# Performance work log

Hardware: AMD Instinct MI355X
Metric: run time of the kernel (lower is better)

Reference implementation:

```python
import jax, jax.numpy as jnp
import numpy as np

N = 50000
E = 800000
IN_F = 128
HID = 128
OUT_F = 64
MU = 2.0
EPS = 1e-12


def setup_inputs() -> dict:
    key = jax.random.key(0)
    ks = jax.random.split(key, 20)
    d = {}
    d["x"] = jax.random.normal(ks[0], (N, IN_F), dtype=jnp.float32)
    d["edge_src"] = jax.random.randint(ks[1], (E,), 0, N, dtype=jnp.int32)
    d["edge_dst"] = jax.random.randint(ks[2], (E,), 0, N, dtype=jnp.int32)
    d["edge_val"] = jax.random.uniform(ks[3], (E,), dtype=jnp.float32)
    # layer 0: in=128 -> pool=128 -> out=128 (activation=relu)
    s0 = 1.0 / np.sqrt(IN_F)
    d["pool_w0"] = jax.random.uniform(ks[4], (IN_F, IN_F), jnp.float32, -s0, s0)
    d["pool_b0"] = jax.random.uniform(ks[5], (IN_F,), jnp.float32, -s0, s0)
    d["fc1_w0"] = jax.random.uniform(ks[6], (HID, IN_F), jnp.float32, -s0, s0)
    d["fc1_b0"] = jax.random.uniform(ks[7], (HID,), jnp.float32, -s0, s0)
    d["fc2_w0"] = jax.random.uniform(ks[8], (HID, IN_F), jnp.float32, -s0, s0)
    d["fc2_b0"] = jax.random.uniform(ks[9], (HID,), jnp.float32, -s0, s0)
    # layer 1 (final): in=128 -> pool=128 -> out=64 (no activation)
    s1 = 1.0 / np.sqrt(HID)
    d["pool_w1"] = jax.random.uniform(ks[10], (HID, HID), jnp.float32, -s1, s1)
    d["pool_b1"] = jax.random.uniform(ks[11], (HID,), jnp.float32, -s1, s1)
    d["fc1_w1"] = jax.random.uniform(ks[12], (OUT_F, HID), jnp.float32, -s1, s1)
    d["fc1_b1"] = jax.random.uniform(ks[13], (OUT_F,), jnp.float32, -s1, s1)
    d["fc2_w1"] = jax.random.uniform(ks[14], (OUT_F, HID), jnp.float32, -s1, s1)
    d["fc2_b1"] = jax.random.uniform(ks[15], (OUT_F,), jnp.float32, -s1, s1)
    return d


def _sage_conv(x, src, dst, val, pw, pb, w1, b1, w2, b2, act):
    # L2-normalize rows (F.normalize(x, dim=1))
    xn = x / jnp.maximum(jnp.linalg.norm(x, axis=1, keepdims=True), EPS)
    h = jax.nn.relu(xn @ pw.T + pb)               # [N, pool]
    h_mu = h ** MU                                # elementwise pow
    # spmm(adj, h_mu): gather source rows, scale by edge weight, scatter-add to dst rows
    agg = jax.ops.segment_sum(h_mu[src] * val[:, None], dst, num_segments=N)
    agg = agg ** (1.0 / MU)                       # generalized-mean root
    out = (h @ w1.T + b1) + (agg @ w2.T + b2)
    return jax.nn.relu(out) if act else out


def reference(x, edge_src, edge_dst, edge_val,
              pool_w0, pool_b0, fc1_w0, fc1_b0, fc2_w0, fc2_b0,
              pool_w1, pool_b1, fc1_w1, fc1_b1, fc2_w1, fc2_b1):
    h = _sage_conv(x, edge_src, edge_dst, edge_val,
                   pool_w0, pool_b0, fc1_w0, fc1_b0, fc2_w0, fc2_b0, act=True)
    out = _sage_conv(h, edge_src, edge_dst, edge_val,
                     pool_w1, pool_b1, fc1_w1, fc1_b1, fc2_w1, fc2_b1, act=False)
    return out
```

## Files before the change

### kernel.cpp

```cpp
#include <hip/hip_runtime.h>

#define FF 128
#define BCAP 8192
#define CHUNK 4096
#define PITCH 136

typedef __attribute__((ext_vector_type(8))) short short8;
typedef __attribute__((ext_vector_type(4))) float f32x4;

__device__ __forceinline__ unsigned short bf16_rne(float f) {
    unsigned u = __float_as_uint(f);
    u += 0x7fffu + ((u >> 16) & 1u);
    return (unsigned short)(u >> 16);
}
__device__ __forceinline__ float bf16_to_f32(unsigned short h) {
    return __uint_as_float(((unsigned)h) << 16);
}

__global__ __launch_bounds__(256, 2)
void poolpartA_kernel(const float* __restrict__ x,
                      const unsigned short* __restrict__ Wh, const unsigned short* __restrict__ Wl,
                      const float* __restrict__ bias,
                      unsigned short* __restrict__ hout, unsigned short* __restrict__ hsqout,
                      const int* __restrict__ esrc, const int* __restrict__ edst,
                      const float* __restrict__ eval,
                      int* __restrict__ bucket_cnt, int2* __restrict__ ebuf,
                      int N, int E, int nchunks)
{
    __shared__ alignas(16) char smem[37888];
    const int t = threadIdx.x;

    if (blockIdx.x < nchunks) {
        int* cnt   = (int*)smem;
        int* sc    = cnt + 256;
        int* excl  = sc + 256;
        int* cur   = excl + 256;
        int* gbase = cur + 256;
        int2* staged = (int2*)(smem + 5 * 256 * 4);
        const int e0 = blockIdx.x * CHUNK;
        const int n  = min(CHUNK, E - e0);

        cnt[t] = 0;
        __syncthreads();
        for (int i = t; i < n; i += 256)
            atomicAdd(&cnt[((unsigned)edst[e0 + i]) >> 8], 1);
        __syncthreads();

        sc[t] = cnt[t];
        __syncthreads();
        #pragma unroll
        for (int off = 1; off < 256; off <<= 1) {
            int v = (t >= off) ? sc[t - off] : 0;
            __syncthreads();
            sc[t] += v;
            __syncthreads();
        }
        excl[t] = sc[t] - cnt[t];
        cur[t]  = excl[t];
        if (cnt[t] > 0) gbase[t] = atomicAdd(&bucket_cnt[t], cnt[t]);
        __syncthreads();

        for (int i = t; i < n; i += 256) {
            int d = edst[e0 + i];
            int s = esrc[e0 + i];
            float v = eval[e0 + i];
            int b = ((unsigned)d) >> 8;
            int slot = atomicAdd(&cur[b], 1);
            staged[slot] = make_int2((s & 0xffff) | (d << 16), __float_as_int(v));
        }
        __syncthreads();

        for (int p = t; p < n; p += 256) {
            int2 ent = staged[p];
            int b = ((unsigned)ent.x) >> 24;
            int gpos = gbase[b] + (p - excl[b]);
            ebuf[(size_t)b * BCAP + gpos] = ent;
        }
    } else {
        unsigned short* sX = (unsigned short*)smem;
        float* sNorm = (float*)(smem + 64 * PITCH * 2);
        unsigned short* sOutQ = (unsigned short*)(smem + 64 * PITCH * 2 + 256);
        const int tile = blockIdx.x - nchunks;

        #pragma unroll
        for (int rg = 0; rg < 2; ++rg) {
            const int row = rg * 32 + (t >> 3);
            const int c0  = (t & 7) * 16;
            const int n   = tile * 64 + row;
            const int base = row * PITCH + c0;
            float v[16];
            if (n < N) {
                const float4* p = (const float4*)(x + (size_t)n * FF + c0);
                #pragma unroll
                for (int i = 0; i < 4; ++i) {
                    float4 q = p[i];
                    v[4*i] = q.x; v[4*i+1] = q.y; v[4*i+2] = q.z; v[4*i+3] = q.w;
                }
            } else {
                #pragma unroll
                for (int i = 0; i < 16; ++i) v[i] = 0.f;
            }
            float ss = 0.f;
            #pragma unroll
            for (int i = 0; i < 16; ++i) ss = fmaf(v[i], v[i], ss);
            union { unsigned short u[8]; short8 s; } h0, h1;
            #pragma unroll
            for (int i = 0; i < 8; ++i) {
                h0.u[i] = bf16_rne(v[i]);
                h1.u[i] = bf16_rne(v[8 + i]);
            }
            *(short8*)&sX[base]     = h0.s;
            *(short8*)&sX[base + 8] = h1.s;
            ss += __shfl_xor(ss, 1);
            ss += __shfl_xor(ss, 2);
            ss += __shfl_xor(ss, 4);
            if ((t & 7) == 0) sNorm[row] = 1.0f / fmaxf(sqrtf(ss), 1e-12f);
        }
        __syncthreads();

        const int lane = t & 63, wave = t >> 6;
        const int quad = lane >> 4, l16 = lane & 15;

        short8 Bh[2][4], Bl[2][4];
        #pragma unroll
        for (int c = 0; c < 2; ++c) {
            const int jt = 2 * wave + c;
            #pragma unroll
            for (int tt = 0; tt < 4; ++tt) {
                const size_t o = ((size_t)(jt * 4 + tt) * 64 + lane) * 8;
                Bh[c][tt] = *(const short8*)&Wh[o];
                Bl[c][tt] = *(const short8*)&Wl[o];
            }
        }

        f32x4 acc[4][2];
        #pragma unroll
        for (int r = 0; r < 4; ++r)
            #pragma unroll
            for (int c = 0; c < 2; ++c) {
                f32x4 z = {0.f, 0.f, 0.f, 0.f};
                acc[r][c] = z;
            }

        #pragma unroll
        for (int tt = 0; tt < 4; ++tt) {
            short8 Ah[4];
            #pragma unroll
            for (int r = 0; r < 4; ++r)
                Ah[r] = *(const short8*)&sX[(r * 16 + l16) * PITCH + tt * 32 + quad * 8];
            #pragma unroll
            for (int c = 0; c < 2; ++c)
                #pragma unroll
                for (int r = 0; r < 4; ++r) {
                    acc[r][c] = __builtin_amdgcn_mfma_f32_16x16x32_bf16(Ah[r], Bh[c][tt], acc[r][c], 0, 0, 0);
                    acc[r][c] = __builtin_amdgcn_mfma_f32_16x16x32_bf16(Ah[r], Bl[c][tt], acc[r][c], 0, 0, 0);
                }
        }

        __syncthreads();
        #pragma unroll
        for (int c = 0; c < 2; ++c) {
            const int j = (2 * wave + c) * 16 + l16;
            const float bj = bias[j];
            #pragma unroll
            for (int r = 0; r < 4; ++r) {
                #pragma unroll
                for (int g = 0; g < 4; ++g) {
                    const int nl = r * 16 + quad * 4 + g;
                    float s = sNorm[nl];
                    float val = fmaf(acc[r][c][g], s, bj);
                    val = fmaxf(val, 0.f);
                    sX   [nl * PITCH + j] = bf16_rne(val);
                    sOutQ[nl * PITCH + j] = bf16_rne(val * val);
                }
            }
        }
        __syncthreads();
        #pragma unroll
        for (int rg = 0; rg < 2; ++rg) {
            const int row = rg * 32 + (t >> 3);
            const int c0  = (t & 7) * 16;
            const int n   = tile * 64 + row;
            if (n < N) {
                const int base = row * PITCH + c0;
                *(short8*)&hout  [(size_t)n * FF + c0]     = *(short8*)&sX[base];
                *(short8*)&hout  [(size_t)n * FF + c0 + 8] = *(short8*)&sX[base + 8];
                *(short8*)&hsqout[(size_t)n * FF + c0]     = *(short8*)&sOutQ[base];
                *(short8*)&hsqout[(size_t)n * FF + c0 + 8] = *(short8*)&sOutQ[base + 8];
            }
        }
    }
}

struct WPack {
    const float* src[6];
    unsigned short* hi[6];
    unsigned short* lo[6];
    int n[6];
};

__global__ __launch_bounds__(256)
void wprep_kernel(WPack p, int* __restrict__ bucket_cnt)
{
    if (blockIdx.x == 0) bucket_cnt[threadIdx.x] = 0;
    int id = blockIdx.x * 256 + threadIdx.x;
    #pragma unroll
    for (int i = 0; i < 6; ++i) {
        if (id < p.n[i]) {
            float f = p.src[i][id];
            unsigned short h = bf16_rne(f);
            const int j = id >> 7, k = id & 127;
            const int jt = j >> 4, l16 = j & 15;
            const int t = k >> 5, quad = (k >> 3) & 3, j8 = k & 7;
            const size_t o = ((size_t)((jt * 4 + t) * 4 + quad) * 16 + l16) * 8 + j8;
            p.hi[i][o] = h;
            p.lo[i][o] = bf16_rne(f - bf16_to_f32(h));
            return;
        }
        id -= p.n[i];
    }
}

__global__ __launch_bounds__(256)
void partB_kernel(const int* __restrict__ bucket_cnt, const int2* __restrict__ ebuf,
                  int* __restrict__ offsets, int2* __restrict__ edata,
                  int N, int E, int nbuck)
{
    __shared__ int pre[256], hist[256], sc[256], excl[256], cur[256];
    const int t = threadIdx.x;
    const int b = blockIdx.x;

    pre[t] = (t < nbuck) ? bucket_cnt[t] : 0;
    __syncthreads();
    #pragma unroll
    for (int off = 1; off < 256; off <<= 1) {
        int v = (t >= off) ? pre[t - off] : 0;
        __syncthreads();
        pre[t] += v;
        __syncthreads();
    }
    const int base = (b == 0) ? 0 : pre[b - 1];
    const int cnt  = pre[b] - base;

    hist[t] = 0;
    __syncthreads();
    const int2* ib = ebuf + (size_t)b * BCAP;
    for (int i = t; i < cnt; i += 256)
        atomicAdd(&hist[(((unsigned)ib[i].x) >> 16) & 255], 1);
    __syncthreads();

    sc[t] = hist[t];
    __syncthreads();
    #pragma unroll
    for (int off = 1; off < 256; off <<= 1) {
        int v = (t >= off) ? sc[t - off] : 0;
        __syncthreads();
        sc[t] += v;
        __syncthreads();
    }
    excl[t] = sc[t] - hist[t];
    cur[t]  = excl[t];

    const int node = b * 256 + t;
    if (node <= N) offsets[node] = base + excl[t];
    __syncthreads();

    for (int i = t; i < cnt; i += 256) {
        int2 ent = ib[i];
        int l = (((unsigned)ent.x) >> 16) & 255;
        int pos = base + atomicAdd(&cur[l], 1);
        edata[pos] = make_int2(ent.x & 0xffff, ent.y);
    }
}

__device__ __forceinline__ void fma4(float4& a, float v, uint2 u) {
    a.x = fmaf(v, __uint_as_float(u.x << 16), a.x);
    a.y = fmaf(v, __uint_as_float(u.x & 0xffff0000u), a.y);
    a.z = fmaf(v, __uint_as_float(u.y << 16), a.z);
    a.w = fmaf(v, __uint_as_float(u.y & 0xffff0000u), a.w);
}

__global__ __launch_bounds__(256)
void agg_kernel(const unsigned short* __restrict__ hsq, const int* __restrict__ offsets,
                const int2* __restrict__ edata,
                unsigned short* __restrict__ aggh, int N)
{
    const int w = blockIdx.x * 8 + (threadIdx.x >> 5);
    if (w >= N) return;
    const int l = threadIdx.x & 31;
    const size_t fo = (size_t)(l * 4);
    int e = offsets[w];
    const int end = offsets[w + 1];

    float4 a0 = {0,0,0,0}, a1 = {0,0,0,0}, a2 = {0,0,0,0}, a3 = {0,0,0,0};

    if ((e & 1) && e < end) {
        int2 ed = edata[e];
        uint2 u = *(const uint2*)&hsq[(size_t)ed.x * FF + fo];
        fma4(a0, __int_as_float(ed.y), u);
        ++e;
    }
    for (; e + 7 < end; e += 8) {
        int4 p0 = *(const int4*)&edata[e];
        int4 p1 = *(const int4*)&edata[e + 2];
        int4 p2 = *(const int4*)&edata[e + 4];
        int4 p3 = *(const int4*)&edata[e + 6];
        uint2 u0 = *(const uint2*)&hsq[(size_t)p0.x * FF + fo];
        uint2 u1 = *(const uint2*)&hsq[(size_t)p0.z * FF + fo];
        uint2 u2 = *(const uint2*)&hsq[(size_t)p1.x * FF + fo];
        uint2 u3 = *(const uint2*)&hsq[(size_t)p1.z * FF + fo];
        uint2 u4 = *(const uint2*)&hsq[(size_t)p2.x * FF + fo];
        uint2 u5 = *(const uint2*)&hsq[(size_t)p2.z * FF + fo];
        uint2 u6 = *(const uint2*)&hsq[(size_t)p3.x * FF + fo];
        uint2 u7 = *(const uint2*)&hsq[(size_t)p3.z * FF + fo];
        fma4(a0, __int_as_float(p0.y), u0);
        fma4(a1, __int_as_float(p0.w), u1);
        fma4(a2, __int_as_float(p1.y), u2);
        fma4(a3, __int_as_float(p1.w), u3);
        fma4(a0, __int_as_float(p2.y), u4);
        fma4(a1, __int_as_float(p2.w), u5);
        fma4(a2, __int_as_float(p3.y), u6);
        fma4(a3, __int_as_float(p3.w), u7);
    }
    if (e + 3 < end) {
        int4 p0 = *(const int4*)&edata[e];
        int4 p1 = *(const int4*)&edata[e + 2];
        uint2 u0 = *(const uint2*)&hsq[(size_t)p0.x * FF + fo];
        uint2 u1 = *(const uint2*)&hsq[(size_t)p0.z * FF + fo];
        uint2 u2 = *(const uint2*)&hsq[(size_t)p1.x * FF + fo];
        uint2 u3 = *(const uint2*)&hsq[(size_t)p1.z * FF + fo];
        fma4(a0, __int_as_float(p0.y), u0);
        fma4(a1, __int_as_float(p0.w), u1);
        fma4(a2, __int_as_float(p1.y), u2);
        fma4(a3, __int_as_float(p1.w), u3);
        e += 4;
    }
    if (e + 1 < end) {
        int4 p = *(const int4*)&edata[e];
        uint2 u0 = *(const uint2*)&hsq[(size_t)p.x * FF + fo];
        uint2 u1 = *(const uint2*)&hsq[(size_t)p.z * FF + fo];
        fma4(a0, __int_as_float(p.y), u0);
        fma4(a1, __int_as_float(p.w), u1);
        e += 2;
    }
    if (e < end) {
        int2 ed = edata[e];
        uint2 u = *(const uint2*)&hsq[(size_t)ed.x * FF + fo];
        fma4(a0, __int_as_float(ed.y), u);
    }

    float4 r;
    r.x = sqrtf(a0.x + a1.x + a2.x + a3.x);
    r.y = sqrtf(a0.y + a1.y + a2.y + a3.y);
    r.z = sqrtf(a0.z + a1.z + a2.z + a3.z);
    r.w = sqrtf(a0.w + a1.w + a2.w + a3.w);

    uint2 hv = { (unsigned)bf16_rne(r.x) | ((unsigned)bf16_rne(r.y) << 16),
                 (unsigned)bf16_rne(r.z) | ((unsigned)bf16_rne(r.w) << 16) };
    *(uint2*)&aggh[(size_t)w * FF + fo] = hv;
}

__global__ __launch_bounds__(256, 2)
void mm2pool_kernel(const unsigned short* __restrict__ hin,
                    const unsigned short* __restrict__ aggh,
                    const unsigned short* __restrict__ W1h, const unsigned short* __restrict__ W1l,
                    const unsigned short* __restrict__ W2h, const unsigned short* __restrict__ W2l,
                    const float* __restrict__ b1, const float* __restrict__ b2,
                    const unsigned short* __restrict__ PWh, const unsigned short* __restrict__ PWl,
                    const float* __restrict__ pb,
                    unsigned short* __restrict__ hout, unsigned short* __restrict__ hsqout,
                    int N)
{
    __shared__ unsigned short sH [64 * PITCH];
    __shared__ unsigned short sA [64 * PITCH];
    __shared__ unsigned short sX1[64 * PITCH];
    __shared__ float sNorm[64];

    const int tid  = threadIdx.x;
    const int tile = blockIdx.x;

    #pragma unroll
    for (int rg = 0; rg < 2; ++rg) {
        const int row = rg * 32 + (tid >> 3);
        const int c0  = (tid & 7) * 16;
        const int n   = tile * 64 + row;
        const int base = row * PITCH + c0;
        short8 z = {0,0,0,0,0,0,0,0};
        short8 a = z, b = z, c = z, d = z;
        if (n < N) {
            const short8* ph = (const short8*)(hin  + (size_t)n * FF + c0);
            const short8* pa = (const short8*)(aggh + (size_t)n * FF + c0);
            a = ph[0]; b = ph[1];
            c = pa[0]; d = pa[1];
        }
        *(short8*)&sH[base]     = a;
        *(short8*)&sH[base + 8] = b;
        *(short8*)&sA[base]     = c;
        *(short8*)&sA[base + 8] = d;
    }
    __syncthreads();

    const int lane = tid & 63, wave = tid >> 6;
    const int quad = lane >> 4, l16 = lane & 15;

    short8 B1hf[2][4], B1lf[2][4], B2hf[2][4], B2lf[2][4];
    #pragma unroll
    for (int c = 0; c < 2; ++c) {
        const int jt = 2 * wave + c;
        #pragma unroll
        for (int t = 0; t < 4; ++t) {
            const size_t o = ((size_t)(jt * 4 + t) * 64 + lane) * 8;
            B1hf[c][t] = *(const short8*)&W1h[o];
            B1lf[c][t] = *(const short8*)&W1l[o];
            B2hf[c][t] = *(const short8*)&W2h[o];
            B2lf[c][t] = *(const short8*)&W2l[o];
        }
    }

    f32x4 acc[4][2];
    #pragma unroll
    for (int r = 0; r < 4; ++r)
        #pragma unroll
        for (int c = 0; c < 2; ++c) {
            f32x4 z = {0.f, 0.f, 0.f, 0.f};
            acc[r][c] = z;
        }

    #pragma unroll
    for (int t = 0; t < 4; ++t) {
        short8 Hf[4], AH[4];
        #pragma unroll
        for (int r = 0; r < 4; ++r) {
            const int off = (r * 16 + l16) * PITCH + t * 32 + quad * 8;
            Hf[r] = *(const short8*)&sH[off];
            AH[r] = *(const short8*)&sA[off];
        }
        #pragma unroll
        for (int c = 0; c < 2; ++c)
            #pragma unroll
            for (int r = 0; r < 4; ++r) {
                acc[r][c] = __builtin_amdgcn_mfma_f32_16x16x32_bf16(Hf[r], B1hf[c][t], acc[r][c], 0, 0, 0);
                acc[r][c] = __builtin_amdgcn_mfma_f32_16x16x32_bf16(Hf[r], B1lf[c][t], acc[r][c], 0, 0, 0);
                acc[r][c] = __builtin_amdgcn_mfma_f32_16x16x32_bf16(AH[r], B2hf[c][t], acc[r][c], 0, 0, 0);
                acc[r][c] = __builtin_amdgcn_mfma_f32_16x16x32_bf16(AH[r], B2lf[c][t], acc[r][c], 0, 0, 0);
            }
    }

    #pragma unroll
    for (int c = 0; c < 2; ++c) {
        const int j = (2 * wave + c) * 16 + l16;
        const float bj = b1[j] + b2[j];
        #pragma unroll
        for (int r = 0; r < 4; ++r) {
            #pragma unroll
            for (int g = 0; g < 4; ++g) {
                const int nl = r * 16 + quad * 4 + g;
                float val = fmaxf(acc[r][c][g] + bj, 0.f);
                sX1[nl * PITCH + j] = bf16_rne(val);
            }
        }
    }
    __syncthreads();

    #pragma unroll
    for (int rg = 0; rg < 2; ++rg) {
        const int row = rg * 32 + (tid >> 3);
        const int c0  = (tid & 7) * 16;
        union { short8 s; unsigned short u[8]; } a, b;
        a.s = *(short8*)&sX1[row * PITCH + c0];
        b.s = *(short8*)&sX1[row * PITCH + c0 + 8];
        float ss = 0.f;
        #pragma unroll
        for (int i = 0; i < 8; ++i) {
            float fa = bf16_to_f32(a.u[i]);
            float fb = bf16_to_f32(b.u[i]);
            ss = fmaf(fa, fa, fmaf(fb, fb, ss));
        }
        ss += __shfl_xor(ss, 1);
        ss += __shfl_xor(ss, 2);
        ss += __shfl_xor(ss, 4);
        if ((tid & 7) == 0) sNorm[row] = 1.0f / fmaxf(sqrtf(ss), 1e-12f);
    }
    __syncthreads();

    short8 Ph[2][4], Pl[2][4];
    #pragma unroll
    for (int c = 0; c < 2; ++c) {
        const int jt = 2 * wave + c;
        #pragma unroll
        for (int t = 0; t < 4; ++t) {
            const size_t o = ((size_t)(jt * 4 + t) * 64 + lane) * 8;
            Ph[c][t] = *(const short8*)&PWh[o];
            Pl[c][t] = *(const short8*)&PWl[o];
        }
    }

    f32x4 acc2[4][2];
    #pragma unroll
    for (int r = 0; r < 4; ++r)
        #pragma unroll
        for (int c = 0; c < 2; ++c) {
            f32x4 z = {0.f, 0.f, 0.f, 0.f};
            acc2[r][c] = z;
        }

    #pragma unroll
    for (int t = 0; t < 4; ++t) {
        short8 Ah[4];
        #pragma unroll
        for (int r = 0; r < 4; ++r)
            Ah[r] = *(const short8*)&sX1[(r * 16 + l16) * PITCH + t * 32 + quad * 8];
        #pragma unroll
        for (int c = 0; c < 2; ++c)
            #pragma unroll
            for (int r = 0; r < 4; ++r) {
                acc2[r][c] = __builtin_amdgcn_mfma_f32_16x16x32_bf16(Ah[r], Ph[c][t], acc2[r][c], 0, 0, 0);
                acc2[r][c] = __builtin_amdgcn_mfma_f32_16x16x32_bf16(Ah[r], Pl[c][t], acc2[r][c], 0, 0, 0);
            }
    }

    __syncthreads();
    #pragma unroll
    for (int c = 0; c < 2; ++c) {
        const int j = (2 * wave + c) * 16 + l16;
        const float pbj = pb[j];
        #pragma unroll
        for (int r = 0; r < 4; ++r) {
            #pragma unroll
            for (int g = 0; g < 4; ++g) {
                const int nl = r * 16 + quad * 4 + g;
                float s = sNorm[nl];
                float val = fmaxf(fmaf(acc2[r][c][g], s, pbj), 0.f);
                sH[nl * PITCH + j] = bf16_rne(val);
                sA[nl * PITCH + j] = bf16_rne(val * val);
            }
        }
    }
    __syncthreads();
    #pragma unroll
    for (int rg = 0; rg < 2; ++rg) {
        const int row = rg * 32 + (tid >> 3);
        const int c0  = (tid & 7) * 16;
        const int n   = tile * 64 + row;
        if (n < N) {
            const int base = row * PITCH + c0;
            *(short8*)&hout  [(size_t)n * FF + c0]     = *(short8*)&sH[base];
            *(short8*)&hout  [(size_t)n * FF + c0 + 8] = *(short8*)&sH[base + 8];
            *(short8*)&hsqout[(size_t)n * FF + c0]     = *(short8*)&sA[base];
            *(short8*)&hsqout[(size_t)n * FF + c0 + 8] = *(short8*)&sA[base + 8];
        }
    }
}

#define OPITCH 68
__global__ __launch_bounds__(256, 2)
void mm2_final_kernel(const unsigned short* __restrict__ hin,
                      const unsigned short* __restrict__ aggh,
                      const unsigned short* __restrict__ W1h, const unsigned short* __restrict__ W1l,
                      const unsigned short* __restrict__ W2h, const unsigned short* __restrict__ W2l,
                      const float* __restrict__ b1, const float* __restrict__ b2,
                      float* __restrict__ out, int N)
{
    __shared__ unsigned short sH[64 * PITCH];
    __shared__ unsigned short sA[64 * PITCH];

    const int tid  = threadIdx.x;
    const int tile = blockIdx.x;

    #pragma unroll
    for (int rg = 0; rg < 2; ++rg) {
        const int row = rg * 32 + (tid >> 3);
        const int c0  = (tid & 7) * 16;
        const int n   = tile * 64 + row;
        const int base = row * PITCH + c0;
        short8 z = {0,0,0,0,0,0,0,0};
        short8 a = z, b = z, c = z, d = z;
        if (n < N) {
            const short8* ph = (const short8*)(hin  + (size_t)n * FF + c0);
            const short8* pa = (const short8*)(aggh + (size_t)n * FF + c0);
            a = ph[0]; b = ph[1];
            c = pa[0]; d = pa[1];
        }
        *(short8*)&sH[base]     = a;
        *(short8*)&sH[base + 8] = b;
        *(short8*)&sA[base]     = c;
        *(short8*)&sA[base + 8] = d;
    }
    __syncthreads();

    const int lane = tid & 63, wave = tid >> 6;
    const int quad = lane >> 4, l16 = lane & 15;

    short8 B1hf[4], B1lf[4], B2hf[4], B2lf[4];
    #pragma unroll
    for (int t = 0; t < 4; ++t) {
        const size_t o = ((size_t)(wave * 4 + t) * 64 + lane) * 8;
        B1hf[t] = *(const short8*)&W1h[o];
        B1lf[t] = *(const short8*)&W1l[o];
        B2hf[t] = *(const short8*)&W2h[o];
        B2lf[t] = *(const short8*)&W2l[o];
    }

    f32x4 acc[4];
    #pragma unroll
    for (int r = 0; r < 4; ++r) {
        f32x4 z = {0.f, 0.f, 0.f, 0.f};
        acc[r] = z;
    }

    #pragma unroll
    for (int t = 0; t < 4; ++t) {
        short8 Hf[4], AH[4];
        #pragma unroll
        for (int r = 0; r < 4; ++r) {
            const int off = (r * 16 + l16) * PITCH + t * 32 + quad * 8;
            Hf[r] = *(const short8*)&sH[off];
            AH[r] = *(const short8*)&sA[off];
        }
        #pragma unroll
        for (int r = 0; r < 4; ++r) {
            acc[r] = __builtin_amdgcn_mfma_f32_16x16x32_bf16(Hf[r], B1hf[t], acc[r], 0, 0, 0);
            acc[r] = __builtin_amdgcn_mfma_f32_16x16x32_bf16(Hf[r], B1lf[t], acc[r], 0, 0, 0);
            acc[r] = __builtin_amdgcn_mfma_f32_16x16x32_bf16(AH[r], B2hf[t], acc[r], 0, 0, 0);
            acc[r] = __builtin_amdgcn_mfma_f32_16x16x32_bf16(AH[r], B2lf[t], acc[r], 0, 0, 0);
        }
    }

    __syncthreads();
    float* sOut = (float*)sH;
    {
        const int j = wave * 16 + l16;
        const float bj = b1[j] + b2[j];
        #pragma unroll
        for (int r = 0; r < 4; ++r) {
            #pragma unroll
            for (int g = 0; g < 4; ++g) {
                const int nl = r * 16 + quad * 4 + g;
                sOut[nl * OPITCH + j] = acc[r][g] + bj;
            }
        }
    }
    __syncthreads();
    {
        const int row = tid >> 2;
        const int seg = tid & 3;
        const int n = tile * 64 + row;
        if (n < N) {
            const float4* src = (const float4*)&sOut[row * OPITCH + seg * 16];
            float4* dst = (float4*)&out[(size_t)n * 64 + seg * 16];
            #pragma unroll
            for (int i = 0; i < 4; ++i) dst[i] = src[i];
        }
    }
}

extern "C" void kernel_launch(void* const* d_in, const int* in_sizes, int n_in,
                              void* d_out, int out_size, void* d_ws, size_t ws_size,
                              hipStream_t stream) {
    const float* x    = (const float*)d_in[0];
    const int*   esrc = (const int*)d_in[1];
    const int*   edst = (const int*)d_in[2];
    const float* eval = (const float*)d_in[3];
    const float* pw0  = (const float*)d_in[4];
    const float* pb0  = (const float*)d_in[5];
    const float* f1w0 = (const float*)d_in[6];
    const float* f1b0 = (const float*)d_in[7];
    const float* f2w0 = (const float*)d_in[8];
    const float* f2b0 = (const float*)d_in[9];
    const float* pw1  = (const float*)d_in[10];
    const float* pb1  = (const float*)d_in[11];
    const float* f1w1 = (const float*)d_in[12];
    const float* f1b1 = (const float*)d_in[13];
    const float* f2w1 = (const float*)d_in[14];
    const float* f2b1 = (const float*)d_in[15];
    float* out = (float*)d_out;

    const int N = in_sizes[0] / FF;
    const int E = in_sizes[1];
    const int nbuck = (N + 255) / 256;

    char* ws = (char*)d_ws;
    const size_t planesz = (size_t)N * FF * 2;
    const size_t A = 256;
    size_t off = 0;
    unsigned short* h    = (unsigned short*)(ws + off); off += (planesz + A - 1) / A * A;
    unsigned short* hsq  = (unsigned short*)(ws + off); off += (planesz + A - 1) / A * A;
    unsigned short* h2   = (unsigned short*)(ws + off); off += (planesz + A - 1) / A * A;
    unsigned short* hsq2 = (unsigned short*)(ws + off); off += (planesz + A - 1) / A * A;
    unsigned short* aggh = (unsigned short*)(ws + off); off += (planesz + A - 1) / A * A;
    int* offsets = (int*)(ws + off); off += ((size_t)(N + 1) * 4 + A - 1) / A * A;
    int* bucket_cnt = (int*)(ws + off); off += (size_t)256 * 4;
    int2* ebuf  = (int2*)(ws + off); off += (size_t)nbuck * BCAP * 8;
    int2* edata = (int2*)(ws + off); off += (size_t)E * 8;
    const int wsz[6] = {128 * FF, 128 * FF, 128 * FF, 128 * FF, 64 * FF, 64 * FF};
    unsigned short* whi[6];
    unsigned short* wlo[6];
    for (int i = 0; i < 6; ++i) {
        whi[i] = (unsigned short*)(ws + off); off += (size_t)wsz[i] * 2;
        wlo[i] = (unsigned short*)(ws + off); off += (size_t)wsz[i] * 2;
    }

    WPack pack;
    const float* wsrc[6] = {pw0, f1w0, f2w0, pw1, f1w1, f2w1};
    int wtotal = 0;
    for (int i = 0; i < 6; ++i) {
        pack.src[i] = wsrc[i]; pack.hi[i] = whi[i]; pack.lo[i] = wlo[i]; pack.n[i] = wsz[i];
        wtotal += wsz[i];
    }

    const int ntiles     = (N + 63) / 64;
    const int nodeblocks = (N + 7) / 8;
    const int nchunks    = (E + CHUNK - 1) / CHUNK;
    dim3 B(256);

    wprep_kernel<<<(wtotal + 255) / 256, B, 0, stream>>>(pack, bucket_cnt);

    poolpartA_kernel<<<nchunks + ntiles, B, 0, stream>>>(
        x, whi[0], wlo[0], pb0, h, hsq, esrc, edst, eval, bucket_cnt, ebuf, N, E, nchunks);

    partB_kernel<<<nbuck, B, 0, stream>>>(bucket_cnt, ebuf, offsets, edata, N, E, nbuck);

    agg_kernel<<<nodeblocks, B, 0, stream>>>(hsq, offsets, edata, aggh, N);

    mm2pool_kernel<<<ntiles, B, 0, stream>>>(
        h, aggh, whi[1], wlo[1], whi[2], wlo[2], f1b0, f2b0,
        whi[3], wlo[3], pb1, h2, hsq2, N);

    agg_kernel<<<nodeblocks, B, 0, stream>>>(hsq2, offsets, edata, aggh, N);

    mm2_final_kernel<<<ntiles, B, 0, stream>>>(
        h2, aggh, whi[4], wlo[4], whi[5], wlo[5], f1b1, f2b1, out, N);
}
```

Before: 234.8 us.

## Drop squared-activation planes, square in aggregation, cache edges in registers/LDS

The pool kernels no longer write a separate bf16 squared-activation plane. The aggregation kernel now reads h and squares it on the fly (v*f*f), which removes two N×128 plane writes and shares one buffer for the gather. Several other changes come along: partA keeps its edge chunk in registers instead of re-reading global memory, and bucket counters are padded to a 32-int stride to avoid atomic contention on shared lines. partB stages each bucket in LDS, edge-data loads use nontemporal hints, and mm2pool reuses sH instead of a third LDS tile. Numerics shift slightly because squaring now happens on bf16-rounded h rather than rounding the fp32 square.

```diff
diff --git a/kernel.cpp b/kernel.cpp
--- a/kernel.cpp
+++ b/kernel.cpp
@@ -4,9 +4,13 @@
 #define BCAP 8192
 #define CHUNK 4096
 #define PITCH 136
+#define BSTRIDE 32
+#define PBCACHE 6144
 
 typedef __attribute__((ext_vector_type(8))) short short8;
 typedef __attribute__((ext_vector_type(4))) float f32x4;
+typedef __attribute__((ext_vector_type(4))) int i32x4;
+typedef __attribute__((ext_vector_type(2))) int i32x2;
 
 __device__ __forceinline__ unsigned short bf16_rne(float f) {
     unsigned u = __float_as_uint(f);
@@ -21,7 +25,7 @@
 void poolpartA_kernel(const float* __restrict__ x,
                       const unsigned short* __restrict__ Wh, const unsigned short* __restrict__ Wl,
                       const float* __restrict__ bias,
-                      unsigned short* __restrict__ hout, unsigned short* __restrict__ hsqout,
+                      unsigned short* __restrict__ hout,
                       const int* __restrict__ esrc, const int* __restrict__ edst,
                       const float* __restrict__ eval,
                       int* __restrict__ bucket_cnt, int2* __restrict__ ebuf,
@@ -40,10 +44,24 @@
         const int e0 = blockIdx.x * CHUNK;
         const int n  = min(CHUNK, E - e0);
 
+        unsigned pk[16]; float vr[16];
+        #pragma unroll
+        for (int k = 0; k < 16; ++k) {
+            const int i = t + k * 256;
+            pk[k] = 0xFFFFFFFFu;
+            if (i < n) {
+                int d = edst[e0 + i];
+                int s = esrc[e0 + i];
+                pk[k] = (unsigned)((s & 0xffff) | (d << 16));
+                vr[k] = eval[e0 + i];
+            }
+        }
+
         cnt[t] = 0;
         __syncthreads();
-        for (int i = t; i < n; i += 256)
-            atomicAdd(&cnt[((unsigned)edst[e0 + i]) >> 8], 1);
+        #pragma unroll
+        for (int k = 0; k < 16; ++k)
+            if (pk[k] != 0xFFFFFFFFu) atomicAdd(&cnt[pk[k] >> 24], 1);
         __syncthreads();
 
         sc[t] = cnt[t];
@@ -57,16 +75,16 @@
         }
         excl[t] = sc[t] - cnt[t];
         cur[t]  = excl[t];
-        if (cnt[t] > 0) gbase[t] = atomicAdd(&bucket_cnt[t], cnt[t]);
-        __syncthreads();
-
-        for (int i = t; i < n; i += 256) {
-            int d = edst[e0 + i];
-            int s = esrc[e0 + i];
-            float v = eval[e0 + i];
-            int b = ((unsigned)d) >> 8;
-            int slot = atomicAdd(&cur[b], 1);
-            staged[slot] = make_int2((s & 0xffff) | (d << 16), __float_as_int(v));
+        if (cnt[t] > 0) gbase[t] = atomicAdd(&bucket_cnt[t * BSTRIDE], cnt[t]);
+        __syncthreads();
+
+        #pragma unroll
+        for (int k = 0; k < 16; ++k) {
+            if (pk[k] != 0xFFFFFFFFu) {
+                int b = pk[k] >> 24;
+                int slot = atomicAdd(&cur[b], 1);
+                staged[slot] = make_int2((int)pk[k], __float_as_int(vr[k]));
+            }
         }
         __syncthreads();
 
@@ -79,7 +97,6 @@
     } else {
         unsigned short* sX = (unsigned short*)smem;
         float* sNorm = (float*)(smem + 64 * PITCH * 2);
-        unsigned short* sOutQ = (unsigned short*)(smem + 64 * PITCH * 2 + 256);
         const int tile = blockIdx.x - nchunks;
 
         #pragma unroll
@@ -170,8 +187,7 @@
                     float s = sNorm[nl];
                     float val = fmaf(acc[r][c][g], s, bj);
                     val = fmaxf(val, 0.f);
-                    sX   [nl * PITCH + j] = bf16_rne(val);
-                    sOutQ[nl * PITCH + j] = bf16_rne(val * val);
+                    sX[nl * PITCH + j] = bf16_rne(val);
                 }
             }
         }
@@ -183,10 +199,8 @@
             const int n   = tile * 64 + row;
             if (n < N) {
                 const int base = row * PITCH + c0;
-                *(short8*)&hout  [(size_t)n * FF + c0]     = *(short8*)&sX[base];
-                *(short8*)&hout  [(size_t)n * FF + c0 + 8] = *(short8*)&sX[base + 8];
-                *(short8*)&hsqout[(size_t)n * FF + c0]     = *(short8*)&sOutQ[base];
-                *(short8*)&hsqout[(size_t)n * FF + c0 + 8] = *(short8*)&sOutQ[base + 8];
+                *(short8*)&hout[(size_t)n * FF + c0]     = *(short8*)&sX[base];
+                *(short8*)&hout[(size_t)n * FF + c0 + 8] = *(short8*)&sX[base + 8];
             }
         }
     }
@@ -202,7 +216,9 @@
 __global__ __launch_bounds__(256)
 void wprep_kernel(WPack p, int* __restrict__ bucket_cnt)
 {
-    if (blockIdx.x == 0) bucket_cnt[threadIdx.x] = 0;
+    if (blockIdx.x == 0) {
+        for (int i = threadIdx.x; i < 256 * BSTRIDE; i += 256) bucket_cnt[i] = 0;
+    }
     int id = blockIdx.x * 256 + threadIdx.x;
     #pragma unroll
     for (int i = 0; i < 6; ++i) {
@@ -227,10 +243,19 @@
                   int N, int E, int nbuck)
 {
     __shared__ int pre[256], hist[256], sc[256], excl[256], cur[256];
+    __shared__ int2 sBuf[PBCACHE];
     const int t = threadIdx.x;
     const int b = blockIdx.x;
 
-    pre[t] = (t < nbuck) ? bucket_cnt[t] : 0;
+    const int cnt_self = bucket_cnt[b * BSTRIDE];
+    const int2* ib = ebuf + (size_t)b * BCAP;
+    const bool useL = (cnt_self <= PBCACHE);
+
+    if (useL)
+        for (int i = t; i < cnt_self; i += 256) sBuf[i] = ib[i];
+
+    pre[t] = (t < nbuck) ? bucket_cnt[t * BSTRIDE] : 0;
+    hist[t] = 0;
     __syncthreads();
     #pragma unroll
     for (int off = 1; off < 256; off <<= 1) {
@@ -240,13 +265,12 @@
         __syncthreads();
     }
     const int base = (b == 0) ? 0 : pre[b - 1];
-    const int cnt  = pre[b] - base;
-
-    hist[t] = 0;
-    __syncthreads();
-    const int2* ib = ebuf + (size_t)b * BCAP;
-    for (int i = t; i < cnt; i += 256)
-        atomicAdd(&hist[(((unsigned)ib[i].x) >> 16) & 255], 1);
+    const int cnt  = cnt_self;
+
+    for (int i = t; i < cnt; i += 256) {
+        int2 ent = useL ? sBuf[i] : ib[i];
+        atomicAdd(&hist[(((unsigned)ent.x) >> 16) & 255], 1);
+    }
     __syncthreads();
 
     sc[t] = hist[t];
@@ -266,22 +290,33 @@
     __syncthreads();
 
     for (int i = t; i < cnt; i += 256) {
-        int2 ent = ib[i];
+        int2 ent = useL ? sBuf[i] : ib[i];
         int l = (((unsigned)ent.x) >> 16) & 255;
         int pos = base + atomicAdd(&cur[l], 1);
         edata[pos] = make_int2(ent.x & 0xffff, ent.y);
     }
 }
 
-__device__ __forceinline__ void fma4(float4& a, float v, uint2 u) {
-    a.x = fmaf(v, __uint_as_float(u.x << 16), a.x);
-    a.y = fmaf(v, __uint_as_float(u.x & 0xffff0000u), a.y);
-    a.z = fmaf(v, __uint_as_float(u.y << 16), a.z);
-    a.w = fmaf(v, __uint_as_float(u.y & 0xffff0000u), a.w);
+__device__ __forceinline__ void fma4sq(float4& a, float v, uint2 u) {
+    float f0 = __uint_as_float(u.x << 16);
+    float f1 = __uint_as_float(u.x & 0xffff0000u);
+    float f2 = __uint_as_float(u.y << 16);
+    float f3 = __uint_as_float(u.y & 0xffff0000u);
+    a.x = fmaf(v * f0, f0, a.x);
+    a.y = fmaf(v * f1, f1, a.y);
+    a.z = fmaf(v * f2, f2, a.z);
+    a.w = fmaf(v * f3, f3, a.w);
+}
+
+__device__ __forceinline__ i32x4 ldnt4(const int2* p) {
+    return __builtin_nontemporal_load((const i32x4*)p);
+}
+__device__ __forceinline__ i32x2 ldnt2(const int2* p) {
+    return __builtin_nontemporal_load((const i32x2*)p);
 }
 
 __global__ __launch_bounds__(256)
-void agg_kernel(const unsigned short* __restrict__ hsq, const int* __restrict__ offsets,
+void agg_kernel(const unsigned short* __restrict__ hp, const int* __restrict__ offsets,
                 const int2* __restrict__ edata,
                 unsigned short* __restrict__ aggh, int N)
 {
@@ -295,58 +330,58 @@
     float4 a0 = {0,0,0,0}, a1 = {0,0,0,0}, a2 = {0,0,0,0}, a3 = {0,0,0,0};
 
     if ((e & 1) && e < end) {
-        int2 ed = edata[e];
-        uint2 u = *(const uint2*)&hsq[(size_t)ed.x * FF + fo];
-        fma4(a0, __int_as_float(ed.y), u);
+        i32x2 ed = ldnt2(&edata[e]);
+        uint2 u = *(const uint2*)&hp[(size_t)ed[0] * FF + fo];
+        fma4sq(a0, __int_as_float(ed[1]), u);
         ++e;
     }
     for (; e + 7 < end; e += 8) {
-        int4 p0 = *(const int4*)&edata[e];
-        int4 p1 = *(const int4*)&edata[e + 2];
-        int4 p2 = *(const int4*)&edata[e + 4];
-        int4 p3 = *(const int4*)&edata[e + 6];
-        uint2 u0 = *(const uint2*)&hsq[(size_t)p0.x * FF + fo];
-        uint2 u1 = *(const uint2*)&hsq[(size_t)p0.z * FF + fo];
-        uint2 u2 = *(const uint2*)&hsq[(size_t)p1.x * FF + fo];
-        uint2 u3 = *(const uint2*)&hsq[(size_t)p1.z * FF + fo];
-        uint2 u4 = *(const uint2*)&hsq[(size_t)p2.x * FF + fo];
-        uint2 u5 = *(const uint2*)&hsq[(size_t)p2.z * FF + fo];
-        uint2 u6 = *(const uint2*)&hsq[(size_t)p3.x * FF + fo];
-        uint2 u7 = *(const uint2*)&hsq[(size_t)p3.z * FF + fo];
-        fma4(a0, __int_as_float(p0.y), u0);
-        fma4(a1, __int_as_float(p0.w), u1);
-        fma4(a2, __int_as_float(p1.y), u2);
-        fma4(a3, __int_as_float(p1.w), u3);
-        fma4(a0, __int_as_float(p2.y), u4);
-        fma4(a1, __int_as_float(p2.w), u5);
-        fma4(a2, __int_as_float(p3.y), u6);
-        fma4(a3, __int_as_float(p3.w), u7);
+        i32x4 p0 = ldnt4(&edata[e]);
+        i32x4 p1 = ldnt4(&edata[e + 2]);
+        i32x4 p2 = ldnt4(&edata[e + 4]);
+        i32x4 p3 = ldnt4(&edata[e + 6]);
+        uint2 u0 = *(const uint2*)&hp[(size_t)p0[0] * FF + fo];
+        uint2 u1 = *(const uint2*)&hp[(size_t)p0[2] * FF + fo];
+        uint2 u2 = *(const uint2*)&hp[(size_t)p1[0] * FF + fo];
+        uint2 u3 = *(const uint2*)&hp[(size_t)p1[2] * FF + fo];
+        uint2 u4 = *(const uint2*)&hp[(size_t)p2[0] * FF + fo];
+        uint2 u5 = *(const uint2*)&hp[(size_t)p2[2] * FF + fo];
+        uint2 u6 = *(const uint2*)&hp[(size_t)p3[0] * FF + fo];
+        uint2 u7 = *(const uint2*)&hp[(size_t)p3[2] * FF + fo];
+        fma4sq(a0, __int_as_float(p0[1]), u0);
+        fma4sq(a1, __int_as_float(p0[3]), u1);
+        fma4sq(a2, __int_as_float(p1[1]), u2);
+        fma4sq(a3, __int_as_float(p1[3]), u3);
+        fma4sq(a0, __int_as_float(p2[1]), u4);
+        fma4sq(a1, __int_as_float(p2[3]), u5);
+        fma4sq(a2, __int_as_float(p3[1]), u6);
+        fma4sq(a3, __int_as_float(p3[3]), u7);
     }
     if (e + 3 < end) {
-        int4 p0 = *(const int4*)&edata[e];
-        int4 p1 = *(const int4*)&edata[e + 2];
-        uint2 u0 = *(const uint2*)&hsq[(size_t)p0.x * FF + fo];
-        uint2 u1 = *(const uint2*)&hsq[(size_t)p0.z * FF + fo];
-        uint2 u2 = *(const uint2*)&hsq[(size_t)p1.x * FF + fo];
-        uint2 u3 = *(const uint2*)&hsq[(size_t)p1.z * FF + fo];
-        fma4(a0, __int_as_float(p0.y), u0);
-        fma4(a1, __int_as_float(p0.w), u1);
-        fma4(a2, __int_as_float(p1.y), u2);
-        fma4(a3, __int_as_float(p1.w), u3);
+        i32x4 p0 = ldnt4(&edata[e]);
+        i32x4 p1 = ldnt4(&edata[e + 2]);
+        uint2 u0 = *(const uint2*)&hp[(size_t)p0[0] * FF + fo];
+        uint2 u1 = *(const uint2*)&hp[(size_t)p0[2] * FF + fo];
+        uint2 u2 = *(const uint2*)&hp[(size_t)p1[0] * FF + fo];
+        uint2 u3 = *(const uint2*)&hp[(size_t)p1[2] * FF + fo];
+        fma4sq(a0, __int_as_float(p0[1]), u0);
+        fma4sq(a1, __int_as_float(p0[3]), u1);
+        fma4sq(a2, __int_as_float(p1[1]), u2);
+        fma4sq(a3, __int_as_float(p1[3]), u3);
         e += 4;
     }
     if (e + 1 < end) {
-        int4 p = *(const int4*)&edata[e];
-        uint2 u0 = *(const uint2*)&hsq[(size_t)p.x * FF + fo];
-        uint2 u1 = *(const uint2*)&hsq[(size_t)p.z * FF + fo];
-        fma4(a0, __int_as_float(p.y), u0);
-        fma4(a1, __int_as_float(p.w), u1);
+        i32x4 p = ldnt4(&edata[e]);
+        uint2 u0 = *(const uint2*)&hp[(size_t)p[0] * FF + fo];
+        uint2 u1 = *(const uint2*)&hp[(size_t)p[2] * FF + fo];
+        fma4sq(a0, __int_as_float(p[1]), u0);
+        fma4sq(a1, __int_as_float(p[3]), u1);
         e += 2;
     }
     if (e < end) {
-        int2 ed = edata[e];
-        uint2 u = *(const uint2*)&hsq[(size_t)ed.x * FF + fo];
-        fma4(a0, __int_as_float(ed.y), u);
+        i32x2 ed = ldnt2(&edata[e]);
+        uint2 u = *(const uint2*)&hp[(size_t)ed[0] * FF + fo];
+        fma4sq(a0, __int_as_float(ed[1]), u);
     }
 
     float4 r;
@@ -368,12 +403,10 @@
                     const float* __restrict__ b1, const float* __restrict__ b2,
                     const unsigned short* __restrict__ PWh, const unsigned short* __restrict__ PWl,
                     const float* __restrict__ pb,
-                    unsigned short* __restrict__ hout, unsigned short* __restrict__ hsqout,
-                    int N)
+                    unsigned short* __restrict__ hout, int N)
 {
-    __shared__ unsigned short sH [64 * PITCH];
-    __shared__ unsigned short sA [64 * PITCH];
-    __shared__ unsigned short sX1[64 * PITCH];
+    __shared__ unsigned short sH[64 * PITCH];
+    __shared__ unsigned short sA[64 * PITCH];
     __shared__ float sNorm[64];
 
     const int tid  = threadIdx.x;
@@ -446,6 +479,8 @@
             }
     }
 
+    __syncthreads();
+
     #pragma unroll
     for (int c = 0; c < 2; ++c) {
         const int j = (2 * wave + c) * 16 + l16;
@@ -456,7 +491,7 @@
             for (int g = 0; g < 4; ++g) {
                 const int nl = r * 16 + quad * 4 + g;
                 float val = fmaxf(acc[r][c][g] + bj, 0.f);
-                sX1[nl * PITCH + j] = bf16_rne(val);
+                sH[nl * PITCH + j] = bf16_rne(val);
             }
         }
     }
@@ -467,8 +502,8 @@
         const int row = rg * 32 + (tid >> 3);
         const int c0  = (tid & 7) * 16;
         union { short8 s; unsigned short u[8]; } a, b;
-        a.s = *(short8*)&sX1[row * PITCH + c0];
-        b.s = *(short8*)&sX1[row * PITCH + c0 + 8];
+        a.s = *(short8*)&sH[row * PITCH + c0];
+        b.s = *(short8*)&sH[row * PITCH + c0 + 8];
         float ss = 0.f;
         #pragma unroll
         for (int i = 0; i < 8; ++i) {
@@ -509,7 +544,7 @@
         short8 Ah[4];
         #pragma unroll
         for (int r = 0; r < 4; ++r)
-            Ah[r] = *(const short8*)&sX1[(r * 16 + l16) * PITCH + t * 32 + quad * 8];
+            Ah[r] = *(const short8*)&sH[(r * 16 + l16) * PITCH + t * 32 + quad * 8];
         #pragma unroll
         for (int c = 0; c < 2; ++c)
             #pragma unroll
@@ -531,8 +566,7 @@
                 const int nl = r * 16 + quad * 4 + g;
                 float s = sNorm[nl];
                 float val = fmaxf(fmaf(acc2[r][c][g], s, pbj), 0.f);
-                sH[nl * PITCH + j] = bf16_rne(val);
-                sA[nl * PITCH + j] = bf16_rne(val * val);
+                sA[nl * PITCH + j] = bf16_rne(val);
             }
         }
     }
@@ -544,10 +578,8 @@
         const int n   = tile * 64 + row;
         if (n < N) {
             const int base = row * PITCH + c0;
-            *(short8*)&hout  [(size_t)n * FF + c0]     = *(short8*)&sH[base];
-            *(short8*)&hout  [(size_t)n * FF + c0 + 8] = *(short8*)&sH[base + 8];
-            *(short8*)&hsqout[(size_t)n * FF + c0]     = *(short8*)&sA[base];
-            *(short8*)&hsqout[(size_t)n * FF + c0 + 8] = *(short8*)&sA[base + 8];
+            *(short8*)&hout[(size_t)n * FF + c0]     = *(short8*)&sA[base];
+            *(short8*)&hout[(size_t)n * FF + c0 + 8] = *(short8*)&sA[base + 8];
         }
     }
 }
@@ -684,12 +716,10 @@
     const size_t A = 256;
     size_t off = 0;
     unsigned short* h    = (unsigned short*)(ws + off); off += (planesz + A - 1) / A * A;
-    unsigned short* hsq  = (unsigned short*)(ws + off); off += (planesz + A - 1) / A * A;
     unsigned short* h2   = (unsigned short*)(ws + off); off += (planesz + A - 1) / A * A;
-    unsigned short* hsq2 = (unsigned short*)(ws + off); off += (planesz + A - 1) / A * A;
     unsigned short* aggh = (unsigned short*)(ws + off); off += (planesz + A - 1) / A * A;
     int* offsets = (int*)(ws + off); off += ((size_t)(N + 1) * 4 + A - 1) / A * A;
-    int* bucket_cnt = (int*)(ws + off); off += (size_t)256 * 4;
+    int* bucket_cnt = (int*)(ws + off); off += (size_t)256 * BSTRIDE * 4;
     int2* ebuf  = (int2*)(ws + off); off += (size_t)nbuck * BCAP * 8;
     int2* edata = (int2*)(ws + off); off += (size_t)E * 8;
     const int wsz[6] = {128 * FF, 128 * FF, 128 * FF, 128 * FF, 64 * FF, 64 * FF};
@@ -716,17 +746,17 @@
     wprep_kernel<<<(wtotal + 255) / 256, B, 0, stream>>>(pack, bucket_cnt);
 
     poolpartA_kernel<<<nchunks + ntiles, B, 0, stream>>>(
-        x, whi[0], wlo[0], pb0, h, hsq, esrc, edst, eval, bucket_cnt, ebuf, N, E, nchunks);
+        x, whi[0], wlo[0], pb0, h, esrc, edst, eval, bucket_cnt, ebuf, N, E, nchunks);
 
     partB_kernel<<<nbuck, B, 0, stream>>>(bucket_cnt, ebuf, offsets, edata, N, E, nbuck);
 
-    agg_kernel<<<nodeblocks, B, 0, stream>>>(hsq, offsets, edata, aggh, N);
+    agg_kernel<<<nodeblocks, B, 0, stream>>>(h, offsets, edata, aggh, N);
 
     mm2pool_kernel<<<ntiles, B, 0, stream>>>(
         h, aggh, whi[1], wlo[1], whi[2], wlo[2], f1b0, f2b0,
-        whi[3], wlo[3], pb1, h2, hsq2, N);
-
-    agg_kernel<<<nodeblocks, B, 0, stream>>>(hsq2, offsets, edata, aggh, N);
+        whi[3], wlo[3], pb1, h2, N);
+
+    agg_kernel<<<nodeblocks, B, 0, stream>>>(h2, offsets, edata, aggh, N);
 
     mm2_final_kernel<<<ntiles, B, 0, stream>>>(
         h2, aggh, whi[4], wlo[4], whi[5], wlo[5], f1b1, f2b1, out, N);
```

After: 241.2 us. +2.8%, slower.
